# Kernel tuning notes

Hardware: AMD Instinct MI355X
Metric: run time of the kernel (lower is better)

Reference implementation:

```python
import jax, jax.numpy as jnp
import numpy as np

B, L, U, G, H = 64, 110, 768, 512, 256
WP = WF = 10
NSP = 2
R = 2 * NSP * NSP      # 8 relation types
NB = 30                # RGCN num_bases
FF = 2048              # torch TransformerEncoderLayer default dim_feedforward
TAG = 7
N = B * L
NEG = -1e9


def _build_edges():
    # static windowed edge structure (all dialogues have length L)
    js, ks = [], []
    for j in range(L):
        for k in range(max(0, j - WP), min(L - 1, j + WF) + 1):
            js.append(j); ks.append(k)
    j = np.asarray(js, np.int32); k = np.asarray(ks, np.int32)
    c = (j >= k).astype(np.int32)  # edge_type suffix: '0' if j<k else '1'
    off = (np.arange(B, dtype=np.int32) * L)[:, None]
    src = (j[None, :] + off).reshape(-1)
    dst = (k[None, :] + off).reshape(-1)
    return src, dst, np.tile(k, B), np.tile(c, B)


def _ln(x, g, b):
    m = x.mean(-1, keepdims=True)
    v = ((x - m) ** 2).mean(-1, keepdims=True)
    return (x - m) / jnp.sqrt(v + 1e-5) * g + b


def _core(x, in_proj_w, in_proj_b, out_proj_w, out_proj_b, ln1_g, ln1_b,
          ff1_w, ff1_b, ff2_w, ff2_b, ln2_g, ln2_b, to_w, to_b, att_w,
          rgcn_basis, rgcn_comp, rgcn_root, rgcn_bias,
          gc_rel_w, gc_rel_b, gc_root_w, clf1_w, clf1_b, clf2_w, clf2_b,
          speaker, src, dst, k_local, cflag):
    # --- SeqContext: 1-layer, 1-head post-norm transformer (eval mode) ---
    qkv = x @ in_proj_w.T + in_proj_b
    q, kk, v = jnp.split(qkv, 3, axis=-1)
    attn = jax.nn.softmax(jnp.einsum('bqd,bkd->bqk', q, kk) / jnp.sqrt(jnp.float32(U)), -1)
    a = jnp.einsum('bqk,bkd->bqd', attn, v) @ out_proj_w.T + out_proj_b
    h = _ln(x + a, ln1_g, ln1_b)
    ff = jax.nn.relu(h @ ff1_w.T + ff1_b) @ ff2_w.T + ff2_b
    h = _ln(h + ff, ln2_g, ln2_b)
    feats = h @ to_w.T + to_b                      # (B, L, G) node features

    # --- EdgeAtt: windowed softmax attention, score[j,k] = x_j^T W x_k ---
    scores = jnp.einsum('bjd,de,bke->bjk', feats, att_w, feats)
    rel = jnp.arange(L)[None, :] - jnp.arange(L)[:, None]
    mask = (rel >= -WP) & (rel <= WF)
    alpha = jax.nn.softmax(jnp.where(mask[None], scores, NEG), -1)  # (B, L, L)

    xf = feats.reshape(N, G)
    edge_norm = alpha.reshape(N, L)[src, k_local]   # alpha[b, j, k] per edge

    # --- edge types from speakers: idx = (s1*NSP + s2)*2 + c ---
    sp = speaker.reshape(N)
    etype = (sp[src] * NSP + sp[dst]) * 2 + cflag

    # --- RGCNConv: basis decomposition, per-(node, relation) mean + root ---
    w_rel = jnp.einsum('rb,bgh->rgh', rgcn_comp, rgcn_basis)   # (R, G, H)
    xproj = jnp.einsum('ng,rgh->rnh', xf, w_rel)               # (R, N, H)
    msg = xproj[etype, src]                                    # (E, H)
    seg = dst * R + etype
    cnt = jax.ops.segment_sum(jnp.ones_like(edge_norm), seg, num_segments=N * R)
    msg = msg / jnp.maximum(cnt[seg], 1.0)[:, None]
    h1 = jax.ops.segment_sum(msg, dst, num_segments=N) + xf @ rgcn_root + rgcn_bias

    # --- GraphConv: sum-aggregate edge-weighted neighbors + root ---
    agg = jax.ops.segment_sum(edge_norm[:, None] * h1[src], dst, num_segments=N)
    h2 = agg @ gc_rel_w.T + gc_rel_b + h1 @ gc_root_w.T

    # --- Classifier (dropout inactive in eval) ---
    z = jnp.concatenate([xf, h2], axis=-1)
    return jax.nn.relu(z @ clf1_w.T + clf1_b) @ clf2_w.T + clf2_b  # (N, TAG)


def setup_inputs():
    key = jax.random.key(0)
    ks = jax.random.split(key, 16)
    def rn(i, shape, scale=0.02):
        return jax.random.normal(ks[i], shape, jnp.float32) * scale
    src, dst, k_local, cflag = _build_edges()
    return {
        'x': jax.random.normal(ks[0], (B, L, U), jnp.float32),
        'in_proj_w': rn(1, (3 * U, U)), 'in_proj_b': jnp.zeros((3 * U,), jnp.float32),
        'out_proj_w': rn(2, (U, U)), 'out_proj_b': jnp.zeros((U,), jnp.float32),
        'ln1_g': jnp.ones((U,), jnp.float32), 'ln1_b': jnp.zeros((U,), jnp.float32),
        'ff1_w': rn(3, (FF, U)), 'ff1_b': jnp.zeros((FF,), jnp.float32),
        'ff2_w': rn(4, (U, FF)), 'ff2_b': jnp.zeros((U,), jnp.float32),
        'ln2_g': jnp.ones((U,), jnp.float32), 'ln2_b': jnp.zeros((U,), jnp.float32),
        'to_w': rn(5, (G, U)), 'to_b': jnp.zeros((G,), jnp.float32),
        'att_w': rn(6, (G, G), 2.0 / (G + G)),
        'rgcn_basis': rn(7, (NB, G, H)), 'rgcn_comp': rn(8, (R, NB), 0.2),
        'rgcn_root': rn(9, (G, H)), 'rgcn_bias': jnp.zeros((H,), jnp.float32),
        'gc_rel_w': rn(10, (H, H)), 'gc_rel_b': jnp.zeros((H,), jnp.float32),
        'gc_root_w': rn(11, (H, H)),
        'clf1_w': rn(12, (H, G + H)), 'clf1_b': jnp.zeros((H,), jnp.float32),
        'clf2_w': rn(13, (TAG, H)), 'clf2_b': jnp.zeros((TAG,), jnp.float32),
        'speaker': jax.random.randint(ks[14], (B, L), 0, NSP, jnp.int32),
        'src': jnp.asarray(src), 'dst': jnp.asarray(dst),
        'k_local': jnp.asarray(k_local), 'cflag': jnp.asarray(cflag),
        'length': L,
    }


def reference(x, in_proj_w, in_proj_b, out_proj_w, out_proj_b, ln1_g, ln1_b,
              ff1_w, ff1_b, ff2_w, ff2_b, ln2_g, ln2_b, to_w, to_b, att_w,
              rgcn_basis, rgcn_comp, rgcn_root, rgcn_bias,
              gc_rel_w, gc_rel_b, gc_root_w, clf1_w, clf1_b, clf2_w, clf2_b,
              speaker, src, dst, k_local, cflag, length):
    return _core(x, in_proj_w, in_proj_b, out_proj_w, out_proj_b, ln1_g, ln1_b,
                 ff1_w, ff1_b, ff2_w, ff2_b, ln2_g, ln2_b, to_w, to_b, att_w,
                 rgcn_basis, rgcn_comp, rgcn_root, rgcn_bias,
                 gc_rel_w, gc_rel_b, gc_root_w, clf1_w, clf1_b, clf2_w, clf2_b,
                 speaker, src, dst, k_local, cflag)
```

## Files before the change

kernel.cpp:

```cpp
#include <hip/hip_runtime.h>
#include <hip/hip_bf16.h>
#include <math.h>

#define L_   110
#define B_   64
#define N_   7040
#define U_   768
#define G_   512
#define H_   256
#define FF_  2048
#define EPB_ 2200
#define NC_  2816

typedef __attribute__((ext_vector_type(4))) float f32x4;
typedef __attribute__((ext_vector_type(8))) short bf16x8;

__device__ __forceinline__ ushort f2b(float f) {
  union { __hip_bfloat16 h; ushort u; } cv;
  cv.h = __float2bfloat16(f);
  return cv.u;
}
__device__ __forceinline__ float b2f(ushort u) {
  union { float f; unsigned int i; } cv; cv.i = ((unsigned int)u) << 16; return cv.f;
}

__device__ __forceinline__ int edge_prefix(int j) {
  if (j <= 10)  return j * 11 + (j * (j - 1)) / 2;
  if (j <= 100) return 155 + (j - 10) * 21;
  return 2045 + ((141 - j) * (j - 100)) / 2;
}

struct Segs7 { const float* in[7]; ushort* out[7]; int n4[7]; };

__global__ __launch_bounds__(256)
void cvtmulti_kernel(Segs7 s)
{
  const int seg = blockIdx.y;
  const int n4 = s.n4[seg];
  const float* __restrict__ in = s.in[seg];
  ushort* __restrict__ out = s.out[seg];
  for (int i = blockIdx.x * 256 + threadIdx.x; i < n4; i += gridDim.x * 256) {
    float4 v = ((const float4*)in)[i];
    ushort4 o;
    o.x = f2b(v.x); o.y = f2b(v.y); o.z = f2b(v.z); o.w = f2b(v.w);
    ((ushort4*)out)[i] = o;
  }
}

__global__ __launch_bounds__(256)
void tcvt_kernel(const float* __restrict__ in, ushort* __restrict__ out,
                 int R, int C, size_t inStride, size_t outStride)
{
  __shared__ float t[32][33];
  const int bt = blockIdx.z;
  const int r0 = blockIdx.y * 32, c0 = blockIdx.x * 32;
  const int tx = threadIdx.x & 31, ty = threadIdx.x >> 5;
  for (int i = ty; i < 32; i += 8)
    t[i][tx] = in[bt * inStride + (size_t)(r0 + i) * C + c0 + tx];
  __syncthreads();
  for (int i = ty; i < 32; i += 8)
    out[bt * outStride + (size_t)(c0 + i) * R + r0 + tx] = f2b(t[tx][i]);
}

__global__ __launch_bounds__(256)
void wrel_kernel(const float* __restrict__ basis, const float* __restrict__ comp,
                 float* __restrict__ wrel)
{
  __shared__ float cs[240];
  const int tid = threadIdx.x;
  if (tid < 240) cs[tid] = comp[tid];
  __syncthreads();
  const int gh = blockIdx.x * 256 + tid;
  float acc[8] = {};
  for (int bb = 0; bb < 30; ++bb) {
    float v = basis[(size_t)bb * (G_ * H_) + gh];
#pragma unroll
    for (int r = 0; r < 8; ++r) acc[r] = fmaf(cs[r * 30 + bb], v, acc[r]);
  }
#pragma unroll
  for (int r = 0; r < 8; ++r) wrel[(size_t)r * (G_ * H_) + gh] = acc[r];
}

__global__ __launch_bounds__(256)
void prepmisc_kernel(const float* __restrict__ rb, const float* __restrict__ rel,
                     const float* __restrict__ root, float* __restrict__ bias,
                     ushort* __restrict__ gccat)
{
  const int i = blockIdx.x * 256 + threadIdx.x;
  if (i < NC_) {
    bias[i] = (i < 2560) ? 0.f : rb[i - 2560];
  } else if (i < NC_ + 65536) {
    const int j = i - NC_;
    const int r = j >> 8, c = j & 255;
    gccat[(size_t)r * 512 + c]       = f2b(rel[j]);
    gccat[(size_t)r * 512 + 256 + c] = f2b(root[j]);
  }
}

template<bool BIAS, bool RELU>
__global__ __launch_bounds__(256)
void mgemm_kernel(const ushort* __restrict__ A, const ushort* __restrict__ B,
                  const float* __restrict__ bias, ushort* __restrict__ Cb,
                  int K, int lda, int ldb, int ldc)
{
  __shared__ ushort sA[128 * 64];
  __shared__ ushort sB[128 * 64];
  const int tid = threadIdx.x;
  const int w = tid >> 6, l = tid & 63;

  const int gx = gridDim.x;
  const int nwg = gx * gridDim.y;
  const int lid = blockIdx.y * gx + blockIdx.x;
  const int q = nwg >> 3, r = nwg & 7;
  const int xcd = lid & 7, pos = lid >> 3;
  const int nlid = (xcd < r ? xcd * (q + 1) : r * (q + 1) + (xcd - r) * q) + pos;
  const int m0 = (nlid / gx) * 128, n0 = (nlid % gx) * 128;

  const int srow = l >> 3, sg = l & 7, rbase = w * 32;
  const int wr = w >> 1, wc = w & 1;
  const int lrow = l & 15, lk = l >> 4;
  const int xm = (l & 7) << 4;
  const int kb0 = (lk * 16) ^ xm;
  int aoff[4], boff[4];
#pragma unroll
  for (int i = 0; i < 4; ++i) {
    aoff[i] = (wr * 64 + i * 16 + lrow) * 128 + kb0;
    boff[i] = (wc * 64 + i * 16 + lrow) * 128 + kb0;
  }

  f32x4 acc[4][4];
#pragma unroll
  for (int i = 0; i < 4; ++i)
#pragma unroll
    for (int j = 0; j < 4; ++j) acc[i][j] = (f32x4){0.f, 0.f, 0.f, 0.f};

#define STAGE(k0)                                                              \
  {                                                                            \
    _Pragma("unroll")                                                          \
    for (int i = 0; i < 4; ++i) {                                              \
      const int trow = rbase + i * 8 + srow;                                   \
      const int koff = (sg * 8) ^ ((trow & 7) << 3);                           \
      const ushort* ga = A + (size_t)(m0 + trow) * lda + (k0) + koff;          \
      const ushort* gb = B + (size_t)(n0 + trow) * ldb + (k0) + koff;          \
      __builtin_amdgcn_global_load_lds(                                        \
          (const __attribute__((address_space(1))) void*)ga,                   \
          (__attribute__((address_space(3))) void*)&sA[(rbase + i * 8) * 64],  \
          16, 0, 0);                                                           \
      __builtin_amdgcn_global_load_lds(                                        \
          (const __attribute__((address_space(1))) void*)gb,                   \
          (__attribute__((address_space(3))) void*)&sB[(rbase + i * 8) * 64],  \
          16, 0, 0);                                                           \
    }                                                                          \
  }

  STAGE(0)
  for (int kt = 0;;) {
    __syncthreads();
#pragma unroll
    for (int h = 0; h < 2; ++h) {
      const int hx = h * 64;
      bf16x8 af[4], bfr[4];
#pragma unroll
      for (int i = 0; i < 4; ++i) {
        af[i]  = *(const bf16x8*)&sA[(aoff[i] ^ hx) >> 1];
        bfr[i] = *(const bf16x8*)&sB[(boff[i] ^ hx) >> 1];
      }
#pragma unroll
      for (int mi = 0; mi < 4; ++mi)
#pragma unroll
        for (int ni = 0; ni < 4; ++ni)
          acc[mi][ni] = __builtin_amdgcn_mfma_f32_16x16x32_bf16(
              af[mi], bfr[ni], acc[mi][ni], 0, 0, 0);
    }
    kt += 64;
    if (kt >= K) break;
    __syncthreads();
    STAGE(kt)
  }
#undef STAGE

  const int orow = m0 + wr * 64 + lk * 4;
  const int ocol = n0 + wc * 64 + lrow;
#pragma unroll
  for (int mi = 0; mi < 4; ++mi) {
#pragma unroll
    for (int r2 = 0; r2 < 4; ++r2) {
      const int row = orow + mi * 16 + r2;
#pragma unroll
      for (int ni = 0; ni < 4; ++ni) {
        const int col = ocol + ni * 16;
        float v = acc[mi][ni][r2];
        if constexpr (BIAS) v += bias[col];
        if constexpr (RELU) v = fmaxf(v, 0.f);
        Cb[(size_t)row * ldc + col] = f2b(v);
      }
    }
  }
}

__global__ __launch_bounds__(256)
void vtrans_kernel(const ushort* __restrict__ qkvb, ushort* __restrict__ vt)
{
  __shared__ ushort t[32][33];
  const int b = blockIdx.z;
  const int r0 = blockIdx.y * 32;
  const int c0 = blockIdx.x * 32;
  const int tx = threadIdx.x & 31, ty = threadIdx.x >> 5;
  for (int i = ty; i < 32; i += 8) {
    const int r = r0 + i;
    t[i][tx] = (r < L_) ? qkvb[((size_t)(b * L_) + r) * 2304 + 1536 + c0 + tx]
                        : (ushort)0;
  }
  __syncthreads();
  for (int i = ty; i < 32; i += 8)
    vt[((size_t)b * 768 + c0 + i) * 128 + r0 + tx] = t[tx][i];
}

__global__ __launch_bounds__(256)
void attnM_kernel(const ushort* __restrict__ qkvb, const ushort* __restrict__ vt,
                  ushort* __restrict__ ctxb)
{
  const int wg = blockIdx.x;
  const int xcd = wg & 7, slot = wg >> 3;
  const int b = xcd * 8 + slot / 7;
  const int qr0 = (slot % 7) * 16;
  const int tid = threadIdx.x, w = tid >> 6, l = tid & 63;
  __shared__ float  sS[16 * 128];
  __shared__ ushort sP[16 * 128];
  const int lrow = l & 15, lq = l >> 4;

  const ushort* Qbase = qkvb + ((size_t)(b * L_) + qr0 + lrow) * 2304 + lq * 8;
  f32x4 accS[2] = {{0.f,0.f,0.f,0.f},{0.f,0.f,0.f,0.f}};
  const int nf0 = w * 2;
  for (int k0 = 0; k0 < 768; k0 += 32) {
    bf16x8 aq = *(const bf16x8*)(Qbase + k0);
#pragma unroll
    for (int f = 0; f < 2; ++f) {
      const int nf = nf0 + f;
      if (nf < 7) {
        const ushort* Kp = qkvb + ((size_t)(b * L_) + nf * 16 + lrow) * 2304
                         + 768 + k0 + lq * 8;
        bf16x8 bk = *(const bf16x8*)Kp;
        accS[f] = __builtin_amdgcn_mfma_f32_16x16x32_bf16(aq, bk, accS[f], 0, 0, 0);
      }
    }
  }
  const float scale = 0.03608439182435161f;
#pragma unroll
  for (int f = 0; f < 2; ++f) {
    const int nf = nf0 + f;
    if (nf < 7) {
#pragma unroll
      for (int r = 0; r < 4; ++r)
        sS[(lq * 4 + r) * 128 + nf * 16 + lrow] = accS[f][r] * scale;
    }
  }
  __syncthreads();

  {
    const int row = w * 4 + lq;
    const int c0 = lrow;
    float m = -1e30f;
    for (int c = c0; c < L_; c += 16) m = fmaxf(m, sS[row * 128 + c]);
#pragma unroll
    for (int off = 8; off; off >>= 1) m = fmaxf(m, __shfl_xor(m, off));
    float pv[7];
    float sum = 0.f;
#pragma unroll
    for (int i = 0; i < 7; ++i) {
      const int c = c0 + i * 16;
      float e = (c < L_) ? __expf(sS[row * 128 + c] - m) : 0.f;
      pv[i] = e; sum += e;
    }
#pragma unroll
    for (int off = 8; off; off >>= 1) sum += __shfl_xor(sum, off);
    const float inv = 1.f / sum;
#pragma unroll
    for (int i = 0; i < 8; ++i) {
      const int c = c0 + i * 16;
      ushort pb = (i < 7 && c < L_) ? f2b(pv[i < 7 ? i : 0] * inv) : (ushort)0;
      const int g = (c >> 3) ^ (row & 7);
      sP[row * 128 + g * 8 + (c & 7)] = pb;
    }
  }
  __syncthreads();

  f32x4 accO[12];
#pragma unroll
  for (int i = 0; i < 12; ++i) accO[i] = (f32x4){0.f, 0.f, 0.f, 0.f};
#pragma unroll
  for (int ks = 0; ks < 4; ++ks) {
    const int k = ks * 32 + lq * 8;
    const int g = (k >> 3) ^ (lrow & 7);
    bf16x8 ap = *(const bf16x8*)&sP[lrow * 128 + g * 8];
#pragma unroll
    for (int i = 0; i < 12; ++i) {
      const int col = w * 192 + i * 16 + lrow;
      bf16x8 bv = *(const bf16x8*)(vt + ((size_t)b * 768 + col) * 128 + k);
      accO[i] = __builtin_amdgcn_mfma_f32_16x16x32_bf16(ap, bv, accO[i], 0, 0, 0);
    }
  }
#pragma unroll
  for (int i = 0; i < 12; ++i) {
    const int col = w * 192 + i * 16 + lrow;
#pragma unroll
    for (int r = 0; r < 4; ++r) {
      const int row = qr0 + lq * 4 + r;
      if (row < L_)
        ctxb[((size_t)b * L_ + row) * 768 + col] = f2b(accO[i][r]);
    }
  }
}

template<bool AF32>
__global__ __launch_bounds__(256)
void ln_kernel(const float* __restrict__ Af, const ushort* __restrict__ Ab,
               const ushort* __restrict__ Bres,
               const float* __restrict__ g, const float* __restrict__ beta,
               ushort* __restrict__ outb)
{
  const int row = blockIdx.x, tid = threadIdx.x;
  const ushort* bp = Bres + (size_t)row * U_;
  float a0, a1, a2;
  if constexpr (AF32) {
    const float* ap = Af + (size_t)row * U_;
    a0 = ap[tid]; a1 = ap[tid + 256]; a2 = ap[tid + 512];
  } else {
    const ushort* ap = Ab + (size_t)row * U_;
    a0 = b2f(ap[tid]); a1 = b2f(ap[tid + 256]); a2 = b2f(ap[tid + 512]);
  }
  float v0 = a0 + b2f(bp[tid]);
  float v1 = a1 + b2f(bp[tid + 256]);
  float v2 = a2 + b2f(bp[tid + 512]);
  float s = v0 + v1 + v2, sq = v0 * v0 + v1 * v1 + v2 * v2;
  __shared__ float red[8];
#pragma unroll
  for (int off = 32; off; off >>= 1) { s += __shfl_xor(s, off); sq += __shfl_xor(sq, off); }
  const int wave = tid >> 6, lane = tid & 63;
  if (lane == 0) { red[wave] = s; red[4 + wave] = sq; }
  __syncthreads();
  if (tid == 0) {
    float ts = red[0] + red[1] + red[2] + red[3];
    float tq = red[4] + red[5] + red[6] + red[7];
    float m = ts * (1.f / 768.f);
    float var = tq * (1.f / 768.f) - m * m;
    red[0] = m; red[1] = 1.f / sqrtf(var + 1e-5f);
  }
  __syncthreads();
  const float m = red[0], inv = red[1];
  ushort* ob = outb + (size_t)row * U_;
  ob[tid]       = f2b((v0 - m) * inv * g[tid]       + beta[tid]);
  ob[tid + 256] = f2b((v1 - m) * inv * g[tid + 256] + beta[tid + 256]);
  ob[tid + 512] = f2b((v2 - m) * inv * g[tid + 512] + beta[tid + 512]);
}

__global__ __launch_bounds__(256)
void graphfront_kernel(const ushort* __restrict__ combo, const ushort* __restrict__ fcat,
                       const int* __restrict__ speaker,
                       ushort* __restrict__ catb, float* __restrict__ edge_norm)
{
  const int tid = threadIdx.x;
  if (blockIdx.x < N_ / 8) {
    const int n = blockIdx.x * 8 + (tid >> 5);
    const int lane = tid & 31;
    const int b = n / L_, k = n - b * L_;
    const int j0 = max(0, k - 10), j1 = min(L_ - 1, k + 10);
    const int spk = speaker[n];
    float inv[4];
    {
      int cn[4] = {0, 0, 0, 0};
      for (int j = j0; j <= j1; ++j)
        cn[speaker[b * L_ + j] * 2 + (j >= k ? 1 : 0)]++;
#pragma unroll
      for (int q = 0; q < 4; ++q) inv[q] = cn[q] ? 1.f / (float)cn[q] : 0.f;
    }
    float acc[8] = {};
    for (int j = j0; j <= j1; ++j) {
      const int spj = speaker[b * L_ + j];
      const int c = (j >= k) ? 1 : 0;
      const int et = (spj * 2 + spk) * 2 + c;
      const float w = inv[spj * 2 + c];
      bf16x8 v = *(const bf16x8*)&combo[(size_t)(b * L_ + j) * NC_ + 512 + et * 256 + lane * 8];
#pragma unroll
      for (int i = 0; i < 8; ++i) acc[i] = fmaf(b2f((ushort)v[i]), w, acc[i]);
    }
    bf16x8 rt = *(const bf16x8*)&combo[(size_t)n * NC_ + 2560 + lane * 8];
    bf16x8 o;
#pragma unroll
    for (int i = 0; i < 8; ++i) o[i] = (short)f2b(acc[i] + b2f((ushort)rt[i]));
    *(bf16x8*)&catb[(size_t)n * 512 + 256 + lane * 8] = o;
  } else {
    const int bj = blockIdx.x - N_ / 8;
    const int b = bj / L_, j = bj - b * L_;
    const int k0 = max(0, j - 10), k1 = min(L_ - 1, j + 10);
    __shared__ float s[32];
    const int wave = tid >> 6, lane = tid & 63;
    float tr[8];
    {
      bf16x8 tv = *(const bf16x8*)&combo[(size_t)bj * NC_ + lane * 8];
#pragma unroll
      for (int i = 0; i < 8; ++i) tr[i] = b2f((ushort)tv[i]);
    }
    for (int k = k0 + wave; k <= k1; k += 4) {
      bf16x8 v = *(const bf16x8*)&fcat[(size_t)(b * L_ + k) * 768 + lane * 8];
      float sc = 0.f;
#pragma unroll
      for (int i = 0; i < 8; ++i) sc = fmaf(b2f((ushort)v[i]), tr[i], sc);
#pragma unroll
      for (int off = 32; off; off >>= 1) sc += __shfl_xor(sc, off);
      if (lane == 0) s[k - k0] = sc;
    }
    __syncthreads();
    if (tid == 0) {
      const int W = k1 - k0 + 1;
      float m = -1e30f;
      for (int t = 0; t < W; ++t) m = fmaxf(m, s[t]);
      float sum = 0.f;
      for (int t = 0; t < W; ++t) { float e = __expf(s[t] - m); s[t] = e; sum += e; }
      const float inv = 1.f / sum;
      const int base = b * EPB_ + edge_prefix(j);
      for (int t = 0; t < W; ++t) edge_norm[base + t] = s[t] * inv;
    }
  }
}

__global__ __launch_bounds__(256)
void gcn_gather2_kernel(const float* __restrict__ edge_norm,
                        ushort* __restrict__ catb)
{
  const int tid = threadIdx.x;
  const int n = blockIdx.x * 8 + (tid >> 5);
  const int lane = tid & 31;
  const int b = n / L_, k = n - b * L_;
  const int j0 = max(0, k - 10), j1 = min(L_ - 1, k + 10);
  float acc[8] = {};
  for (int j = j0; j <= j1; ++j) {
    const float w = edge_norm[b * EPB_ + edge_prefix(j) + (k - max(0, j - 10))];
    bf16x8 v = *(const bf16x8*)&catb[(size_t)(b * L_ + j) * 512 + 256 + lane * 8];
#pragma unroll
    for (int i = 0; i < 8; ++i) acc[i] = fmaf(b2f((ushort)v[i]), w, acc[i]);
  }
  bf16x8 o;
#pragma unroll
  for (int i = 0; i < 8; ++i) o[i] = (short)f2b(acc[i]);
  *(bf16x8*)&catb[(size_t)n * 512 + lane * 8] = o;
}

__global__ __launch_bounds__(256)
void clf2_kernel(const ushort* __restrict__ hid, const float* __restrict__ w,
                 const float* __restrict__ bias, float* __restrict__ out)
{
  __shared__ float wsm[7 * H_];
  const int tid = threadIdx.x;
  for (int i = tid; i < 7 * H_; i += 256) wsm[i] = w[i];
  __syncthreads();
  const int idx = blockIdx.x * 256 + threadIdx.x;
  if (idx < N_ * 7) {
    const int n = idx / 7, t = idx - n * 7;
    const ushort* hp = hid + (size_t)n * H_;
    const float* wp = wsm + t * H_;
    float acc = bias[t];
    for (int d0 = 0; d0 < H_; d0 += 8) {
      bf16x8 v = *(const bf16x8*)(hp + d0);
#pragma unroll
      for (int i = 0; i < 8; ++i) acc = fmaf(b2f((ushort)v[i]), wp[d0 + i], acc);
    }
    out[idx] = acc;
  }
}

extern "C" void kernel_launch(void* const* d_in, const int* in_sizes, int n_in,
                              void* d_out, int out_size, void* d_ws, size_t ws_size,
                              hipStream_t stream)
{
  const float* x          = (const float*)d_in[0];
  const float* in_proj_w  = (const float*)d_in[1];
  const float* in_proj_b  = (const float*)d_in[2];
  const float* out_proj_w = (const float*)d_in[3];
  const float* out_proj_b = (const float*)d_in[4];
  const float* ln1_g      = (const float*)d_in[5];
  const float* ln1_b      = (const float*)d_in[6];
  const float* ff1_w      = (const float*)d_in[7];
  const float* ff1_b      = (const float*)d_in[8];
  const float* ff2_w      = (const float*)d_in[9];
  const float* ff2_b      = (const float*)d_in[10];
  const float* ln2_g      = (const float*)d_in[11];
  const float* ln2_b      = (const float*)d_in[12];
  const float* to_w       = (const float*)d_in[13];
  const float* to_b       = (const float*)d_in[14];
  const float* att_w      = (const float*)d_in[15];
  const float* rgcn_basis = (const float*)d_in[16];
  const float* rgcn_comp  = (const float*)d_in[17];
  const float* rgcn_root  = (const float*)d_in[18];
  const float* rgcn_bias  = (const float*)d_in[19];
  const float* gc_rel_w   = (const float*)d_in[20];
  const float* gc_rel_b   = (const float*)d_in[21];
  const float* gc_root_w  = (const float*)d_in[22];
  const float* clf1_w     = (const float*)d_in[23];
  const float* clf1_b     = (const float*)d_in[24];
  const float* clf2_w     = (const float*)d_in[25];
  const float* clf2_b     = (const float*)d_in[26];
  const int*   speaker    = (const int*)d_in[27];
  float* out = (float*)d_out;
  char* p = (char*)d_ws;

  float*  R1f    = (float*)p;
  ushort* R1b    = (ushort*)p;
  p += (size_t)N_ * 2304 * 4;
  ushort* aprojB = (ushort*)p;
  ushort* ffoB   = aprojB;
  float*  en     = (float*)(p + (size_t)N_ * 512 * 4);
  p += (size_t)N_ * 768 * 4;
  ushort* vt    = (ushort*)p;
  ushort* hidB  = (ushort*)p;
  p += (size_t)N_ * 768 * 4;
  ushort* xb    = (ushort*)p;
  ushort* ctxb  = xb;
  p += (size_t)N_ * 768 * 2;
  ushort* hb    = (ushort*)p;
  ushort* catb  = hb;
  p += (size_t)N_ * 768 * 2;
  ushort* fcat  = (ushort*)p; p += (size_t)N_ * 768 * 2;
  ushort* in_projb = (ushort*)p; p += (size_t)2304 * 768 * 2;
  ushort* out_projb= (ushort*)p; p += (size_t)768 * 768 * 2;
  ushort* ff1b     = (ushort*)p; p += (size_t)2048 * 768 * 2;
  ushort* ff2b     = (ushort*)p; p += (size_t)768 * 2048 * 2;
  ushort* tob      = (ushort*)p; p += (size_t)512 * 768 * 2;
  ushort* combw    = (ushort*)p; p += (size_t)NC_ * 512 * 2;
  ushort* gccat    = (ushort*)p; p += (size_t)256 * 512 * 2;
  ushort* clf1b16  = (ushort*)p; p += (size_t)256 * 768 * 2;
  float*  bias_comb= (float*)p;  p += NC_ * 4;
  float*  wrelTmp  = R1f;

  Segs7 segs;
  segs.in[0] = x;          segs.out[0] = xb;        segs.n4[0] = N_ * 768 / 4;
  segs.in[1] = in_proj_w;  segs.out[1] = in_projb;  segs.n4[1] = 2304 * 768 / 4;
  segs.in[2] = out_proj_w; segs.out[2] = out_projb; segs.n4[2] = 768 * 768 / 4;
  segs.in[3] = ff1_w;      segs.out[3] = ff1b;      segs.n4[3] = 2048 * 768 / 4;
  segs.in[4] = ff2_w;      segs.out[4] = ff2b;      segs.n4[4] = 768 * 2048 / 4;
  segs.in[5] = to_w;       segs.out[5] = tob;       segs.n4[5] = 512 * 768 / 4;
  segs.in[6] = clf1_w;     segs.out[6] = clf1b16;   segs.n4[6] = 256 * 768 / 4;
  cvtmulti_kernel<<<dim3(768, 7), 256, 0, stream>>>(segs);
  prepmisc_kernel<<<(NC_ + 65536 + 255) / 256, 256, 0, stream>>>(
      rgcn_bias, gc_rel_w, gc_root_w, bias_comb, gccat);
  tcvt_kernel<<<dim3(16, 16, 1), 256, 0, stream>>>(att_w, combw, 512, 512, 0, 0);
  wrel_kernel<<<512, 256, 0, stream>>>(rgcn_basis, rgcn_comp, wrelTmp);
  tcvt_kernel<<<dim3(8, 16, 8), 256, 0, stream>>>(wrelTmp, combw + (size_t)512 * 512,
                                                  512, 256,
                                                  (size_t)512 * 256, (size_t)256 * 512);
  tcvt_kernel<<<dim3(8, 16, 1), 256, 0, stream>>>(rgcn_root, combw + (size_t)2560 * 512,
                                                  512, 256, 0, 0);

  mgemm_kernel<true, false><<<dim3(18, 55), 256, 0, stream>>>(
      xb, in_projb, in_proj_b, R1b, 768, 768, 768, 2304);
  vtrans_kernel<<<dim3(24, 4, 64), 256, 0, stream>>>(R1b, vt);
  attnM_kernel<<<448, 256, 0, stream>>>(R1b, vt, ctxb);
  mgemm_kernel<true, false><<<dim3(6, 55), 256, 0, stream>>>(
      ctxb, out_projb, out_proj_b, aprojB, 768, 768, 768, 768);
  ln_kernel<true><<<N_, 256, 0, stream>>>(x, nullptr, aprojB, ln1_g, ln1_b, hb);
  mgemm_kernel<true, true><<<dim3(16, 55), 256, 0, stream>>>(
      hb, ff1b, ff1_b, R1b, 768, 768, 768, 2048);
  mgemm_kernel<true, false><<<dim3(6, 55), 256, 0, stream>>>(
      R1b, ff2b, ff2_b, ffoB, 2048, 2048, 2048, 768);
  ln_kernel<false><<<N_, 256, 0, stream>>>(nullptr, hb, ffoB, ln2_g, ln2_b, hb);
  mgemm_kernel<true, false><<<dim3(4, 55), 256, 0, stream>>>(
      hb, tob, to_b, fcat, 768, 768, 768, 768);
  mgemm_kernel<true, false><<<dim3(22, 55), 256, 0, stream>>>(
      fcat, combw, bias_comb, R1b, 512, 768, 512, NC_);
  graphfront_kernel<<<N_ / 8 + N_, 256, 0, stream>>>(R1b, fcat, speaker, catb, en);
  gcn_gather2_kernel<<<N_ / 8, 256, 0, stream>>>(en, catb);
  mgemm_kernel<true, false><<<dim3(2, 55), 256, 0, stream>>>(
      catb, gccat, gc_rel_b, fcat + 512, 512, 512, 512, 768);
  mgemm_kernel<true, true><<<dim3(2, 55), 256, 0, stream>>>(
      fcat, clf1b16, clf1_b, hidB, 768, 768, 768, 256);
  clf2_kernel<<<(N_ * 7 + 255) / 256, 256, 0, stream>>>(hidB, clf2_w, clf2_b, out);
}
```

Baseline: 322.2 us.

## Add 128x64 GEMM tile for narrow-N GEMMs and merge prep kernels

Adds a 128x64-tile variant of the bf16 MFMA GEMM and uses it for the GEMMs with small N (out_proj, ff2, to, gc, clf1). This doubles the workgroup count on the 256-CU GPU, where grids of 110-330 blocks underfill the device. It also fuses the weight-conversion and prep kernels and the three transpose-convert launches into fewer launches to cut launch overhead. Smaller tiles mean less reuse of each A tile and more redundant A loads.

After: 303.7 us. 1.06x faster.

```diff
diff --git a/kernel.cpp b/kernel.cpp
--- a/kernel.cpp
+++ b/kernel.cpp
@@ -33,33 +33,56 @@
 struct Segs7 { const float* in[7]; ushort* out[7]; int n4[7]; };
 
 __global__ __launch_bounds__(256)
-void cvtmulti_kernel(Segs7 s)
+void cvtprep_kernel(Segs7 s, const float* __restrict__ rb,
+                    const float* __restrict__ rel, const float* __restrict__ root,
+                    float* __restrict__ bias, ushort* __restrict__ gccat)
 {
   const int seg = blockIdx.y;
-  const int n4 = s.n4[seg];
-  const float* __restrict__ in = s.in[seg];
-  ushort* __restrict__ out = s.out[seg];
-  for (int i = blockIdx.x * 256 + threadIdx.x; i < n4; i += gridDim.x * 256) {
-    float4 v = ((const float4*)in)[i];
-    ushort4 o;
-    o.x = f2b(v.x); o.y = f2b(v.y); o.z = f2b(v.z); o.w = f2b(v.w);
-    ((ushort4*)out)[i] = o;
-  }
-}
-
-__global__ __launch_bounds__(256)
-void tcvt_kernel(const float* __restrict__ in, ushort* __restrict__ out,
-                 int R, int C, size_t inStride, size_t outStride)
-{
+  if (seg < 7) {
+    const int n4 = s.n4[seg];
+    const float* __restrict__ in = s.in[seg];
+    ushort* __restrict__ out = s.out[seg];
+    for (int i = blockIdx.x * 256 + threadIdx.x; i < n4; i += gridDim.x * 256) {
+      float4 v = ((const float4*)in)[i];
+      ushort4 o;
+      o.x = f2b(v.x); o.y = f2b(v.y); o.z = f2b(v.z); o.w = f2b(v.w);
+      ((ushort4*)out)[i] = o;
+    }
+  } else {
+    const int i = blockIdx.x * 256 + threadIdx.x;
+    if (i < NC_) {
+      bias[i] = (i < 2560) ? 0.f : rb[i - 2560];
+    } else if (i < NC_ + 65536) {
+      const int j = i - NC_;
+      const int r = j >> 8, c = j & 255;
+      gccat[(size_t)r * 512 + c]       = f2b(rel[j]);
+      gccat[(size_t)r * 512 + 256 + c] = f2b(root[j]);
+    }
+  }
+}
+
+__global__ __launch_bounds__(256)
+void tcvt3_kernel(const float* __restrict__ attw, const float* __restrict__ wrelTmp,
+                  const float* __restrict__ root, ushort* __restrict__ combw)
+{
+  const int z = blockIdx.z;
+  const float* in;
+  ushort* out;
+  int C;
+  if (z == 0)      { in = attw; out = combw; C = 512; }
+  else if (z <= 8) { if (blockIdx.x >= 8) return;
+                     in = wrelTmp + (size_t)(z - 1) * 512 * 256;
+                     out = combw + (size_t)(512 + (z - 1) * 256) * 512; C = 256; }
+  else             { if (blockIdx.x >= 8) return;
+                     in = root; out = combw + (size_t)2560 * 512; C = 256; }
   __shared__ float t[32][33];
-  const int bt = blockIdx.z;
   const int r0 = blockIdx.y * 32, c0 = blockIdx.x * 32;
   const int tx = threadIdx.x & 31, ty = threadIdx.x >> 5;
   for (int i = ty; i < 32; i += 8)
-    t[i][tx] = in[bt * inStride + (size_t)(r0 + i) * C + c0 + tx];
+    t[i][tx] = in[(size_t)(r0 + i) * C + c0 + tx];
   __syncthreads();
   for (int i = ty; i < 32; i += 8)
-    out[bt * outStride + (size_t)(c0 + i) * R + r0 + tx] = f2b(t[tx][i]);
+    out[(size_t)(c0 + i) * 512 + r0 + tx] = f2b(t[tx][i]);
 }
 
 __global__ __launch_bounds__(256)
@@ -79,22 +102,6 @@
   }
 #pragma unroll
   for (int r = 0; r < 8; ++r) wrel[(size_t)r * (G_ * H_) + gh] = acc[r];
-}
-
-__global__ __launch_bounds__(256)
-void prepmisc_kernel(const float* __restrict__ rb, const float* __restrict__ rel,
-                     const float* __restrict__ root, float* __restrict__ bias,
-                     ushort* __restrict__ gccat)
-{
-  const int i = blockIdx.x * 256 + threadIdx.x;
-  if (i < NC_) {
-    bias[i] = (i < 2560) ? 0.f : rb[i - 2560];
-  } else if (i < NC_ + 65536) {
-    const int j = i - NC_;
-    const int r = j >> 8, c = j & 255;
-    gccat[(size_t)r * 512 + c]       = f2b(rel[j]);
-    gccat[(size_t)r * 512 + 256 + c] = f2b(root[j]);
-  }
 }
 
 template<bool BIAS, bool RELU>
@@ -183,6 +190,109 @@
   const int ocol = n0 + wc * 64 + lrow;
 #pragma unroll
   for (int mi = 0; mi < 4; ++mi) {
+#pragma unroll
+    for (int r2 = 0; r2 < 4; ++r2) {
+      const int row = orow + mi * 16 + r2;
+#pragma unroll
+      for (int ni = 0; ni < 4; ++ni) {
+        const int col = ocol + ni * 16;
+        float v = acc[mi][ni][r2];
+        if constexpr (BIAS) v += bias[col];
+        if constexpr (RELU) v = fmaxf(v, 0.f);
+        Cb[(size_t)row * ldc + col] = f2b(v);
+      }
+    }
+  }
+}
+
+template<bool BIAS, bool RELU>
+__global__ __launch_bounds__(256)
+void mgemm64_kernel(const ushort* __restrict__ A, const ushort* __restrict__ B,
+                    const float* __restrict__ bias, ushort* __restrict__ Cb,
+                    int K, int lda, int ldb, int ldc)
+{
+  __shared__ ushort sA[128 * 64];
+  __shared__ ushort sB[64 * 64];
+  const int tid = threadIdx.x;
+  const int w = tid >> 6, l = tid & 63;
+
+  const int gx = gridDim.x;
+  const int nwg = gx * gridDim.y;
+  const int lid = blockIdx.y * gx + blockIdx.x;
+  const int q = nwg >> 3, r = nwg & 7;
+  const int xcd = lid & 7, pos = lid >> 3;
+  const int nlid = (xcd < r ? xcd * (q + 1) : r * (q + 1) + (xcd - r) * q) + pos;
+  const int m0 = (nlid / gx) * 128, n0 = (nlid % gx) * 64;
+
+  const int srow = l >> 3, sg = l & 7;
+  const int lrow = l & 15, lk = l >> 4;
+  const int xm = (l & 7) << 4;
+  const int kb0 = (lk * 16) ^ xm;
+  int aoff[2], boff[4];
+#pragma unroll
+  for (int i = 0; i < 2; ++i) aoff[i] = (w * 32 + i * 16 + lrow) * 128 + kb0;
+#pragma unroll
+  for (int i = 0; i < 4; ++i) boff[i] = (i * 16 + lrow) * 128 + kb0;
+
+  f32x4 acc[2][4];
+#pragma unroll
+  for (int i = 0; i < 2; ++i)
+#pragma unroll
+    for (int j = 0; j < 4; ++j) acc[i][j] = (f32x4){0.f, 0.f, 0.f, 0.f};
+
+#define STAGE64(k0)                                                            \
+  {                                                                            \
+    _Pragma("unroll")                                                          \
+    for (int i = 0; i < 4; ++i) {                                              \
+      const int trow = w * 32 + i * 8 + srow;                                  \
+      const int koff = (sg * 8) ^ ((trow & 7) << 3);                           \
+      const ushort* ga = A + (size_t)(m0 + trow) * lda + (k0) + koff;          \
+      __builtin_amdgcn_global_load_lds(                                        \
+          (const __attribute__((address_space(1))) void*)ga,                   \
+          (__attribute__((address_space(3))) void*)&sA[(w * 32 + i * 8) * 64], \
+          16, 0, 0);                                                           \
+    }                                                                          \
+    _Pragma("unroll")                                                          \
+    for (int i = 0; i < 2; ++i) {                                              \
+      const int trow = w * 16 + i * 8 + srow;                                  \
+      const int koff = (sg * 8) ^ ((trow & 7) << 3);                           \
+      const ushort* gb = B + (size_t)(n0 + trow) * ldb + (k0) + koff;          \
+      __builtin_amdgcn_global_load_lds(                                        \
+          (const __attribute__((address_space(1))) void*)gb,                   \
+          (__attribute__((address_space(3))) void*)&sB[(w * 16 + i * 8) * 64], \
+          16, 0, 0);                                                           \
+    }                                                                          \
+  }
+
+  STAGE64(0)
+  for (int kt = 0;;) {
+    __syncthreads();
+#pragma unroll
+    for (int h = 0; h < 2; ++h) {
+      const int hx = h * 64;
+      bf16x8 af[2], bfr[4];
+#pragma unroll
+      for (int i = 0; i < 2; ++i) af[i] = *(const bf16x8*)&sA[(aoff[i] ^ hx) >> 1];
+#pragma unroll
+      for (int i = 0; i < 4; ++i) bfr[i] = *(const bf16x8*)&sB[(boff[i] ^ hx) >> 1];
+#pragma unroll
+      for (int mi = 0; mi < 2; ++mi)
+#pragma unroll
+        for (int ni = 0; ni < 4; ++ni)
+          acc[mi][ni] = __builtin_amdgcn_mfma_f32_16x16x32_bf16(
+              af[mi], bfr[ni], acc[mi][ni], 0, 0, 0);
+    }
+    kt += 64;
+    if (kt >= K) break;
+    __syncthreads();
+    STAGE64(kt)
+  }
+#undef STAGE64
+
+  const int orow = m0 + w * 32 + lk * 4;
+  const int ocol = n0 + lrow;
+#pragma unroll
+  for (int mi = 0; mi < 2; ++mi) {
 #pragma unroll
     for (int r2 = 0; r2 < 4; ++r2) {
       const int row = orow + mi * 16 + r2;
@@ -540,38 +650,32 @@
   segs.in[4] = ff2_w;      segs.out[4] = ff2b;      segs.n4[4] = 768 * 2048 / 4;
   segs.in[5] = to_w;       segs.out[5] = tob;       segs.n4[5] = 512 * 768 / 4;
   segs.in[6] = clf1_w;     segs.out[6] = clf1b16;   segs.n4[6] = 256 * 768 / 4;
-  cvtmulti_kernel<<<dim3(768, 7), 256, 0, stream>>>(segs);
-  prepmisc_kernel<<<(NC_ + 65536 + 255) / 256, 256, 0, stream>>>(
-      rgcn_bias, gc_rel_w, gc_root_w, bias_comb, gccat);
-  tcvt_kernel<<<dim3(16, 16, 1), 256, 0, stream>>>(att_w, combw, 512, 512, 0, 0);
+  cvtprep_kernel<<<dim3(768, 8), 256, 0, stream>>>(
+      segs, rgcn_bias, gc_rel_w, gc_root_w, bias_comb, gccat);
   wrel_kernel<<<512, 256, 0, stream>>>(rgcn_basis, rgcn_comp, wrelTmp);
-  tcvt_kernel<<<dim3(8, 16, 8), 256, 0, stream>>>(wrelTmp, combw + (size_t)512 * 512,
-                                                  512, 256,
-                                                  (size_t)512 * 256, (size_t)256 * 512);
-  tcvt_kernel<<<dim3(8, 16, 1), 256, 0, stream>>>(rgcn_root, combw + (size_t)2560 * 512,
-                                                  512, 256, 0, 0);
+  tcvt3_kernel<<<dim3(16, 16, 10), 256, 0, stream>>>(att_w, wrelTmp, rgcn_root, combw);
 
   mgemm_kernel<true, false><<<dim3(18, 55), 256, 0, stream>>>(
       xb, in_projb, in_proj_b, R1b, 768, 768, 768, 2304);
   vtrans_kernel<<<dim3(24, 4, 64), 256, 0, stream>>>(R1b, vt);
   attnM_kernel<<<448, 256, 0, stream>>>(R1b, vt, ctxb);
-  mgemm_kernel<true, false><<<dim3(6, 55), 256, 0, stream>>>(
+  mgemm64_kernel<true, false><<<dim3(12, 55), 256, 0, stream>>>(
       ctxb, out_projb, out_proj_b, aprojB, 768, 768, 768, 768);
   ln_kernel<true><<<N_, 256, 0, stream>>>(x, nullptr, aprojB, ln1_g, ln1_b, hb);
   mgemm_kernel<true, true><<<dim3(16, 55), 256, 0, stream>>>(
       hb, ff1b, ff1_b, R1b, 768, 768, 768, 2048);
-  mgemm_kernel<true, false><<<dim3(6, 55), 256, 0, stream>>>(
+  mgemm64_kernel<true, false><<<dim3(12, 55), 256, 0, stream>>>(
       R1b, ff2b, ff2_b, ffoB, 2048, 2048, 2048, 768);
   ln_kernel<false><<<N_, 256, 0, stream>>>(nullptr, hb, ffoB, ln2_g, ln2_b, hb);
-  mgemm_kernel<true, false><<<dim3(4, 55), 256, 0, stream>>>(
+  mgemm64_kernel<true, false><<<dim3(8, 55), 256, 0, stream>>>(
       hb, tob, to_b, fcat, 768, 768, 768, 768);
   mgemm_kernel<true, false><<<dim3(22, 55), 256, 0, stream>>>(
       fcat, combw, bias_comb, R1b, 512, 768, 512, NC_);
   graphfront_kernel<<<N_ / 8 + N_, 256, 0, stream>>>(R1b, fcat, speaker, catb, en);
   gcn_gather2_kernel<<<N_ / 8, 256, 0, stream>>>(en, catb);
-  mgemm_kernel<true, false><<<dim3(2, 55), 256, 0, stream>>>(
+  mgemm64_kernel<true, false><<<dim3(4, 55), 256, 0, stream>>>(
       catb, gccat, gc_rel_b, fcat + 512, 512, 512, 512, 768);
-  mgemm_kernel<true, true><<<dim3(2, 55), 256, 0, stream>>>(
+  mgemm64_kernel<true, true><<<dim3(4, 55), 256, 0, stream>>>(
       fcat, clf1b16, clf1_b, hidB, 768, 768, 768, 256);
   clf2_kernel<<<(N_ * 7 + 255) / 256, 256, 0, stream>>>(hidB, clf2_w, clf2_b, out);
 }
```
